# Performance work log

Hardware: AMD Instinct MI355X
Metric: run time of the kernel (lower is better)

Reference implementation:

```python
import jax, jax.numpy as jnp
import numpy as np

B, L, D = 2, 2048, 768
H = 12
HD = D // H  # 64
SCALE = HD ** -0.5


def setup_inputs() -> dict:
    key = jax.random.key(0)
    k1, k2, k3 = jax.random.split(key, 3)
    x = jax.random.normal(k1, (B, L, D), dtype=jnp.float32)
    mask = jnp.ones((B, L), dtype=jnp.int32)
    # nn.Linear weights: [out_features, in_features]
    Wqkv = jax.random.normal(k2, (3 * D, D), dtype=jnp.float32) * (D ** -0.5)
    bqkv = jnp.zeros((3 * D,), dtype=jnp.float32)
    Wout = jax.random.normal(k3, (D, D), dtype=jnp.float32) * (D ** -0.5)
    bout = jnp.zeros((D,), dtype=jnp.float32)
    return {"x": x, "mask": mask, "Wqkv": Wqkv, "bqkv": bqkv, "Wout": Wout, "bout": bout}


def reference(x, mask, Wqkv, bqkv, Wout, bout):
    Bx, Lx, Dx = x.shape
    # qkv projection: [B,L,3D] -> [3,B,H,L,HD]
    qkv = x @ Wqkv.T + bqkv
    qkv = qkv.reshape(Bx, Lx, 3, H, HD).transpose(2, 0, 3, 1, 4)
    q, k, v = qkv[0], qkv[1], qkv[2]
    # scores [B,H,L,L]
    attn = jnp.einsum('bhqd,bhkd->bhqk', q, k) * SCALE
    attn = jnp.where(mask[:, None, None, :] == 0, -jnp.inf, attn)
    attn = jax.nn.softmax(attn, axis=-1)
    # dropout p=0.0 -> identity
    out = jnp.einsum('bhqk,bhkd->bhqd', attn, v)
    out = out.transpose(0, 2, 1, 3).reshape(Bx, Lx, Dx)
    return out @ Wout.T + bout
```

## Files before the change

kernel.cpp:

```cpp
#include <hip/hip_runtime.h>
#include <hip/hip_bf16.h>

#define DEV __device__ __forceinline__

typedef __bf16 bf16_t;
typedef bf16_t bf16x8 __attribute__((ext_vector_type(8)));
typedef float f32x4 __attribute__((ext_vector_type(4)));
typedef float f32x16 __attribute__((ext_vector_type(16)));
typedef unsigned int u32x4 __attribute__((ext_vector_type(4)));

constexpr int Bc = 2, Lc = 2048, Dc = 768, Hc = 12, HDc = 64;
constexpr int NTOK = Bc * Lc;
constexpr int QKVN = 3 * Dc;
constexpr float ATT_SCALE = 0.125f;
constexpr float LOG2E = 1.44269504088896f;

DEV unsigned short f2bf(float f) {
  unsigned int u = __builtin_bit_cast(unsigned int, f);
  u += 0x7FFFu + ((u >> 16) & 1u);
  return (unsigned short)(u >> 16);
}

DEV bf16x8 ld16(const unsigned short* p) {
  return __builtin_bit_cast(bf16x8, *reinterpret_cast<const u32x4*>(p));
}

DEV unsigned cvtpk(float lo, float hi) {
  unsigned r;
  asm("v_cvt_pk_bf16_f32 %0, %1, %2" : "=v"(r) : "v"(lo), "v"(hi));
  return r;
}

DEV void gload16(const unsigned short* g, unsigned short* l) {
  __builtin_amdgcn_global_load_lds(
      (const __attribute__((address_space(1))) unsigned int*)g,
      (__attribute__((address_space(3))) unsigned int*)l, 16, 0, 0);
}

__global__ __launch_bounds__(256) void prep_kernel(
    const float* __restrict__ x, const float* __restrict__ Wqkv,
    const float* __restrict__ Wout, const int* __restrict__ mask,
    unsigned short* __restrict__ xb, unsigned short* __restrict__ wqkvb,
    unsigned short* __restrict__ woutb, float* __restrict__ mb,
    int* __restrict__ mflag) {
  const int bid = blockIdx.x, tid = threadIdx.x;
  const float* src; unsigned short* dst; int base;
  if (bid < 3072)      { src = x;    dst = xb;    base = bid; }
  else if (bid < 4800) { src = Wqkv; dst = wqkvb; base = bid - 3072; }
  else if (bid < 5376) { src = Wout; dst = woutb; base = bid - 4800; }
  else {
    int i = (bid - 5376) * 256 + tid;
    int mv = mask[i];
    mb[i] = mv ? 0.f : -1e30f;
    unsigned long long anyz = __ballot(mv == 0);
    if ((tid & 63) == 0) mflag[i >> 6] = (anyz != 0ull) ? 1 : 0;
    return;
  }
  int i = (base * 256 + tid) * 4;
  float4 v = *reinterpret_cast<const float4*>(src + i);
  ushort4 o;
  o.x = f2bf(v.x); o.y = f2bf(v.y); o.z = f2bf(v.z); o.w = f2bf(v.w);
  *reinterpret_cast<ushort4*>(dst + i) = o;
}

template <int MODE>
__global__ __launch_bounds__(256) void gemm_bt(
    const unsigned short* __restrict__ A,
    const unsigned short* __restrict__ Bw,
    const float* __restrict__ bias,
    unsigned short* __restrict__ qb, unsigned short* __restrict__ kb,
    unsigned short* __restrict__ vtb,
    float* __restrict__ Y,
    int M, int N, int K) {
  constexpr int BM = 128, BN = 128, BK = 64;
  __shared__ alignas(16) unsigned short a_lds[BM * BK];
  __shared__ alignas(16) unsigned short b_lds[BN * BK];
  __shared__ alignas(16) unsigned short qk_patch[(MODE == 0) ? 4 : 1][16][72];

  const int tid = threadIdx.x;
  const int lane = tid & 63;
  const int l15 = lane & 15, lg = lane >> 4;
  const int wave = tid >> 6;
  const int wr = wave >> 1, wc = wave & 1;

  const int ntiles = N / BN;
  const int m0 = (blockIdx.x / ntiles) * BM;
  const int n0 = (blockIdx.x % ntiles) * BN;

  f32x4 acc[4][4] = {};

  for (int k0 = 0; k0 < K; k0 += BK) {
#pragma unroll
    for (int i = 0; i < 4; ++i) {
      int cc = i * 256 + tid;
      int row = cc >> 3, col = (cc & 7) * 8;
      gload16(A + (size_t)(m0 + row) * K + k0 + col, &a_lds[(i * 256 + wave * 64) * 8]);
      gload16(Bw + (size_t)(n0 + row) * K + k0 + col, &b_lds[(i * 256 + wave * 64) * 8]);
    }
    __syncthreads();
#pragma unroll
    for (int kk = 0; kk < 2; ++kk) {
      bf16x8 af[4], bfr[4];
#pragma unroll
      for (int m = 0; m < 4; ++m) {
        int row = wr * 64 + m * 16 + l15;
        af[m] = ld16(&a_lds[row * BK + kk * 32 + lg * 8]);
      }
#pragma unroll
      for (int n = 0; n < 4; ++n) {
        int row = wc * 64 + n * 16 + l15;
        bfr[n] = ld16(&b_lds[row * BK + kk * 32 + lg * 8]);
      }
#pragma unroll
      for (int m = 0; m < 4; ++m)
#pragma unroll
        for (int n = 0; n < 4; ++n)
          acc[m][n] = __builtin_amdgcn_mfma_f32_16x16x32_bf16(af[m], bfr[n], acc[m][n], 0, 0, 0);
    }
    __syncthreads();
  }

  if constexpr (MODE == 0) {
    const int base_col = n0 + wc * 64;
    const int s = base_col / Dc;
    const int h = (base_col % Dc) >> 6;
    if (s == 2) {
#pragma unroll
      for (int m = 0; m < 4; ++m) {
        int lq = m0 + wr * 64 + m * 16 + lg * 4;
        int b = lq >> 11, lql = lq & 2047;
#pragma unroll
        for (int n = 0; n < 4; ++n) {
          int d = n * 16 + l15;
          float bv = bias[base_col + n * 16 + l15];
          ushort4 o;
#pragma unroll
          for (int j = 0; j < 4; ++j)
            ((unsigned short*)&o)[j] = f2bf(acc[m][n][j] + bv);
          *reinterpret_cast<ushort4*>(
              vtb + ((size_t)(b * Hc + h) * HDc + d) * Lc + lql) = o;
        }
      }
    } else {
      unsigned short* dst = (s == 0) ? qb : kb;
      const float sc = (s == 0) ? (ATT_SCALE * LOG2E) : 1.0f;
#pragma unroll
      for (int m = 0; m < 4; ++m) {
#pragma unroll
        for (int n = 0; n < 4; ++n) {
          float bv = bias[base_col + n * 16 + l15];
#pragma unroll
          for (int j = 0; j < 4; ++j)
            qk_patch[wave][lg * 4 + j][n * 16 + l15] =
                f2bf((acc[m][n][j] + bv) * sc);
        }
#pragma unroll
        for (int i = 0; i < 2; ++i) {
          int task = i * 64 + lane;
          int r = task >> 3, ch = task & 7;
          int lq = m0 + wr * 64 + m * 16 + r;
          int b = lq >> 11, lql = lq & 2047;
          u32x4 v = *reinterpret_cast<const u32x4*>(&qk_patch[wave][r][ch * 8]);
          *reinterpret_cast<u32x4*>(
              dst + ((size_t)(b * Hc + h) * Lc + lql) * HDc + ch * 8) = v;
        }
      }
    }
  } else {
#pragma unroll
    for (int m = 0; m < 4; ++m) {
      int row_base = m0 + wr * 64 + m * 16 + lg * 4;
#pragma unroll
      for (int n = 0; n < 4; ++n) {
        int col = n0 + wc * 64 + n * 16 + l15;
        float bv = bias[col];
#pragma unroll
        for (int j = 0; j < 4; ++j)
          Y[(size_t)(row_base + j) * Dc + col] = acc[m][n][j] + bv;
      }
    }
  }
}

__global__ __launch_bounds__(256) void attn_kernel(
    const unsigned short* __restrict__ qb,
    const unsigned short* __restrict__ kb,
    const unsigned short* __restrict__ vtb,
    const float* __restrict__ mb,
    const int* __restrict__ mflag,
    unsigned short* __restrict__ aout) {
  __shared__ alignas(16) unsigned short k_lds[2][4096];
  __shared__ alignas(16) unsigned short v_lds[2][4096];
  __shared__ float l_lds[2][32];
  const int tid = threadIdx.x;
  const int lane = tid & 63;
  const int l31 = lane & 31;
  const int hi = lane >> 5;
  const int wave = tid >> 6;
  const int ws = wave & 1;
  const int g = wave >> 1;
  const int f = blockIdx.x;
  const int loc = f >> 3;
  const int bh = (f & 7) * 3 + (loc >> 5);
  const int b = bh / Hc, h = bh % Hc;
  const int q0 = (loc & 31) * 64 + ws * 32;

  const unsigned short* Kbh = kb + (size_t)bh * Lc * HDc;
  const unsigned short* Vbh = vtb + (size_t)bh * HDc * Lc;
  const float* mbb = mb + b * Lc + hi * 4;
  const int* mfp = mflag + b * (Lc / 64);

  bf16x8 qf[4];
  {
    const unsigned short* Qp = qb + ((size_t)bh * Lc + q0 + l31) * HDc + hi * 8;
#pragma unroll
    for (int c = 0; c < 4; ++c) qf[c] = ld16(Qp + c * 16);
  }

  f32x16 accO[2] = {};
  float l_run = 0.f;

#define STAGE(buf, kv0abs)                                                            \
  {                                                                                   \
    _Pragma("unroll")                                                                 \
    for (int jj = 0; jj < 2; ++jj) {                                                  \
      int j = wave * 2 + jj;                                                          \
      int r8 = j * 8 + (lane >> 3);                                                   \
      int csw = (((lane & 7) ^ (lane >> 3) ^ (j & 3))) << 3;                          \
      gload16(Kbh + (size_t)((kv0abs) + r8) * HDc + csw, &k_lds[buf][j * 512]);       \
      gload16(Vbh + (size_t)r8 * Lc + (kv0abs) + csw, &v_lds[buf][j * 512]);          \
    }                                                                                 \
  }

  STAGE(0, 0)
  __syncthreads();

  const int swz = ((l31 & 7) ^ (l31 >> 3)) << 3;

  constexpr int NSTEP = Lc / 64;
  for (int t = 0; t < NSTEP; ++t) {
    const int cur = t & 1;
    if (t + 1 < NSTEP) STAGE(cur ^ 1, (t + 1) * 64)
    const unsigned short* kl = &k_lds[cur][0];
    const unsigned short* vl = &v_lds[cur][0];

    f32x16 s = {};
    __builtin_amdgcn_s_setprio(1);
#pragma unroll
    for (int c = 0; c < 4; ++c) {
      int ch = (((c * 2 + hi) << 3) ^ swz);
      s = __builtin_amdgcn_mfma_f32_32x32x16_bf16(
          ld16(kl + (g * 32 + l31) * 64 + ch), qf[c], s, 0, 0, 0);
    }
    __builtin_amdgcn_s_setprio(0);
    const int kvt = t * 64 + g * 32;
    if (mfp[t]) {
#pragma unroll
      for (int gg = 0; gg < 4; ++gg) {
        float4 m0v = *reinterpret_cast<const float4*>(mbb + kvt + gg * 8);
        s[gg * 4 + 0] += m0v.x; s[gg * 4 + 1] += m0v.y;
        s[gg * 4 + 2] += m0v.z; s[gg * 4 + 3] += m0v.w;
      }
    }
    float rs0 = 0.f, rs1 = 0.f, rs2 = 0.f, rs3 = 0.f;
#pragma unroll
    for (int i = 0; i < 16; i += 4) {
      s[i] = __builtin_amdgcn_exp2f(s[i]);         rs0 += s[i];
      s[i + 1] = __builtin_amdgcn_exp2f(s[i + 1]); rs1 += s[i + 1];
      s[i + 2] = __builtin_amdgcn_exp2f(s[i + 2]); rs2 += s[i + 2];
      s[i + 3] = __builtin_amdgcn_exp2f(s[i + 3]); rs3 += s[i + 3];
    }
    float rs = (rs0 + rs1) + (rs2 + rs3);
    rs += __shfl_xor(rs, 32);
    l_run += rs;
    bf16x8 pf[2];
#pragma unroll
    for (int c = 0; c < 2; ++c) {
      const int o = c * 8;
      unsigned pk01 = cvtpk(s[o + 0], s[o + 1]);
      unsigned pk23 = cvtpk(s[o + 2], s[o + 3]);
      unsigned pk45 = cvtpk(s[o + 4], s[o + 5]);
      unsigned pk67 = cvtpk(s[o + 6], s[o + 7]);
      asm("v_permlane32_swap_b32 %0, %1" : "+v"(pk01), "+v"(pk45));
      asm("v_permlane32_swap_b32 %0, %1" : "+v"(pk23), "+v"(pk67));
      u32x4 w = {pk01, pk23, pk45, pk67};
      pf[c] = __builtin_bit_cast(bf16x8, w);
    }
    __builtin_amdgcn_s_setprio(1);
#pragma unroll
    for (int dt = 0; dt < 2; ++dt) {
#pragma unroll
      for (int c = 0; c < 2; ++c) {
        int ch = (((g * 4 + c * 2 + hi) << 3) ^ swz);
        accO[dt] = __builtin_amdgcn_mfma_f32_32x32x16_bf16(
            ld16(vl + (dt * 32 + l31) * 64 + ch), pf[c], accO[dt], 0, 0, 0);
      }
    }
    __builtin_amdgcn_s_setprio(0);
    __syncthreads();
  }

  float* mO = (float*)&k_lds[0][0];
  if (g == 1) {
#pragma unroll
    for (int dt = 0; dt < 2; ++dt)
#pragma unroll
      for (int i = 0; i < 16; ++i)
        mO[(ws * 32 + dt * 16 + i) * 64 + lane] = accO[dt][i];
    if (hi == 0) l_lds[ws][l31] = l_run;
  }
  __syncthreads();
  if (g == 0) {
    float rl = 1.0f / (l_run + l_lds[ws][l31]);
    const int q = q0 + l31;
    unsigned short* op = aout + ((size_t)(b * Lc + q)) * Dc + h * HDc;
#pragma unroll
    for (int dt = 0; dt < 2; ++dt)
#pragma unroll
      for (int gg = 0; gg < 4; ++gg) {
        ushort4 o;
#pragma unroll
        for (int j = 0; j < 4; ++j) {
          int i = gg * 4 + j;
          float v = (accO[dt][i] + mO[(ws * 32 + dt * 16 + i) * 64 + lane]) * rl;
          ((unsigned short*)&o)[j] = f2bf(v);
        }
        *reinterpret_cast<ushort4*>(op + dt * 32 + gg * 8 + hi * 4) = o;
      }
  }
}

extern "C" void kernel_launch(void* const* d_in, const int* in_sizes, int n_in,
                              void* d_out, int out_size, void* d_ws, size_t ws_size,
                              hipStream_t stream) {
  const float* x    = (const float*)d_in[0];
  const int*   mask = (const int*)d_in[1];
  const float* Wqkv = (const float*)d_in[2];
  const float* bqkv = (const float*)d_in[3];
  const float* Wout = (const float*)d_in[4];
  const float* bout = (const float*)d_in[5];
  float* out = (float*)d_out;

  constexpr size_t NX   = (size_t)NTOK * Dc;
  constexpr size_t NWQ  = (size_t)QKVN * Dc;
  constexpr size_t NWO  = (size_t)Dc * Dc;
  unsigned short* w = (unsigned short*)d_ws;
  unsigned short* xb    = w;            w += NX;
  unsigned short* wqkvb = w;            w += NWQ;
  unsigned short* woutb = w;            w += NWO;
  unsigned short* qbuf  = w;            w += NX;
  unsigned short* kbuf  = w;            w += NX;
  unsigned short* vtb   = w;            w += NX;
  unsigned short* aoutb = w;            w += NX;
  float* mbf = (float*)w;               w += 2 * NTOK;
  int* mflag = (int*)w;

  prep_kernel<<<5392, 256, 0, stream>>>(x, Wqkv, Wout, mask, xb, wqkvb, woutb, mbf, mflag);

  gemm_bt<0><<<(NTOK / 128) * (QKVN / 128), 256, 0, stream>>>(
      xb, wqkvb, bqkv, qbuf, kbuf, vtb, nullptr, NTOK, QKVN, Dc);

  attn_kernel<<<dim3(768), 256, 0, stream>>>(qbuf, kbuf, vtb, mbf, mflag, aoutb);

  gemm_bt<1><<<(NTOK / 128) * (Dc / 128), 256, 0, stream>>>(
      aoutb, woutb, bout, nullptr, nullptr, nullptr, out, NTOK, Dc, Dc);
}
```

Measured before the change: 113.6 us.

## Triple-buffer K/V staging with vmcnt waits and one barrier per step

```diff
diff --git a/kernel.cpp b/kernel.cpp
--- a/kernel.cpp
+++ b/kernel.cpp
@@ -189,8 +189,8 @@
     const float* __restrict__ mb,
     const int* __restrict__ mflag,
     unsigned short* __restrict__ aout) {
-  __shared__ alignas(16) unsigned short k_lds[2][4096];
-  __shared__ alignas(16) unsigned short v_lds[2][4096];
+  __shared__ alignas(16) unsigned short k_lds[3][4096];
+  __shared__ alignas(16) unsigned short v_lds[3][4096];
   __shared__ float l_lds[2][32];
   const int tid = threadIdx.x;
   const int lane = tid & 63;
@@ -210,6 +210,12 @@
   const float* mbb = mb + b * Lc + hi * 4;
   const int* mfp = mflag + b * (Lc / 64);
 
+  unsigned long long mbits;
+  {
+    int mv = (lane < 32) ? mfp[lane] : 0;
+    mbits = __ballot(mv != 0);
+  }
+
   bf16x8 qf[4];
   {
     const unsigned short* Qp = qb + ((size_t)bh * Lc + q0 + l31) * HDc + hi * 8;
@@ -220,29 +226,45 @@
   f32x16 accO[2] = {};
   float l_run = 0.f;
 
-#define STAGE(buf, kv0abs)                                                            \
-  {                                                                                   \
-    _Pragma("unroll")                                                                 \
-    for (int jj = 0; jj < 2; ++jj) {                                                  \
-      int j = wave * 2 + jj;                                                          \
-      int r8 = j * 8 + (lane >> 3);                                                   \
-      int csw = (((lane & 7) ^ (lane >> 3) ^ (j & 3))) << 3;                          \
-      gload16(Kbh + (size_t)((kv0abs) + r8) * HDc + csw, &k_lds[buf][j * 512]);       \
-      gload16(Vbh + (size_t)r8 * Lc + (kv0abs) + csw, &v_lds[buf][j * 512]);          \
-    }                                                                                 \
-  }
-
-  STAGE(0, 0)
-  __syncthreads();
+  const int j0 = wave * 2, j1 = j0 + 1;
+  const int r80 = j0 * 8 + (lane >> 3), r81 = r80 + 8;
+  const int csw0 = (((lane & 7) ^ (lane >> 3) ^ (j0 & 3))) << 3;
+  const int csw1 = (((lane & 7) ^ (lane >> 3) ^ (j1 & 3))) << 3;
+  const unsigned short* kp0 = Kbh + (size_t)r80 * HDc + csw0;
+  const unsigned short* kp1 = Kbh + (size_t)r81 * HDc + csw1;
+  const unsigned short* vp0 = Vbh + (size_t)r80 * Lc + csw0;
+  const unsigned short* vp1 = Vbh + (size_t)r81 * Lc + csw1;
+
+#define STAGE(buf)                                \
+  {                                               \
+    gload16(kp0, &k_lds[buf][j0 * 512]);          \
+    gload16(kp1, &k_lds[buf][j1 * 512]);          \
+    gload16(vp0, &v_lds[buf][j0 * 512]);          \
+    gload16(vp1, &v_lds[buf][j1 * 512]);          \
+    kp0 += 64 * HDc; kp1 += 64 * HDc;             \
+    vp0 += 64; vp1 += 64;                         \
+  }
+
+  STAGE(0)
+  STAGE(1)
 
   const int swz = ((l31 & 7) ^ (l31 >> 3)) << 3;
 
   constexpr int NSTEP = Lc / 64;
+  int cs = 0;
   for (int t = 0; t < NSTEP; ++t) {
-    const int cur = t & 1;
-    if (t + 1 < NSTEP) STAGE(cur ^ 1, (t + 1) * 64)
-    const unsigned short* kl = &k_lds[cur][0];
-    const unsigned short* vl = &v_lds[cur][0];
+    if (t < NSTEP - 1) {
+      asm volatile("s_waitcnt vmcnt(4)" ::: "memory");
+    } else {
+      asm volatile("s_waitcnt vmcnt(0)" ::: "memory");
+    }
+    __builtin_amdgcn_s_barrier();
+    __builtin_amdgcn_sched_barrier(0);
+    int ss = cs + 2; if (ss >= 3) ss -= 3;
+    if (t + 2 < NSTEP) STAGE(ss)
+
+    const unsigned short* kl = &k_lds[cs][0];
+    const unsigned short* vl = &v_lds[cs][0];
 
     f32x16 s = {};
     __builtin_amdgcn_s_setprio(1);
@@ -253,8 +275,8 @@
           ld16(kl + (g * 32 + l31) * 64 + ch), qf[c], s, 0, 0, 0);
     }
     __builtin_amdgcn_s_setprio(0);
-    const int kvt = t * 64 + g * 32;
-    if (mfp[t]) {
+    if ((mbits >> t) & 1ull) {
+      const int kvt = t * 64 + g * 32;
 #pragma unroll
       for (int gg = 0; gg < 4; ++gg) {
         float4 m0v = *reinterpret_cast<const float4*>(mbb + kvt + gg * 8);
@@ -297,9 +319,10 @@
       }
     }
     __builtin_amdgcn_s_setprio(0);
-    __syncthreads();
-  }
-
+    ++cs; if (cs == 3) cs = 0;
+  }
+
+  __syncthreads();
   float* mO = (float*)&k_lds[0][0];
   if (g == 1) {
 #pragma unroll
```

Result: no change. 115.0 us (+1.3%).
